# Kernel optimization log

Measured on AMD Instinct MI355X. Metric: run time of the kernel, lower is better.

The kernel has to match this reference:

```python
import jax, jax.numpy as jnp
import numpy as np
import math

N, H, E, G = 20000, 256, 320000, 1000
NF, NS = 64, 3           # sinusoid frequencies, spatial dims
DIS = 2 * NF * NS        # 384
EIN = 2 * H + 9 + DIS    # edge MLP input dim = 905


def silu(x):
    return x * jax.nn.sigmoid(x)


def sin_emb(x):
    # x: [E, 3] -> [E, 2*NF*3]
    freqs = 2.0 * math.pi * jnp.arange(NF, dtype=x.dtype)
    emb = (x[..., None] * freqs).reshape(x.shape[0], NF * NS)
    return jnp.concatenate([jnp.sin(emb), jnp.cos(emb)], axis=-1)


def layer_norm(x, gamma, beta, eps=1e-5):
    mu = jnp.mean(x, axis=-1, keepdims=True)
    var = jnp.var(x, axis=-1, keepdims=True)
    return (x - mu) * jax.lax.rsqrt(var + eps) * gamma + beta


def setup_inputs() -> dict:
    key = jax.random.key(0)
    ks = jax.random.split(key, 16)
    s = 0.02
    return {
        "node_features": jax.random.normal(ks[0], (N, H), jnp.float32),
        "lattices": jax.random.normal(ks[1], (G, 3, 3), jnp.float32),
        "edge_index": jax.random.randint(ks[2], (2, E), 0, N, dtype=jnp.int64),
        "edge2graph": jnp.sort(jax.random.randint(ks[3], (E,), 0, G, dtype=jnp.int64)),
        "frac_diff": jax.random.uniform(ks[4], (E, NS), jnp.float32),
        "num_atoms": jax.random.randint(ks[5], (G,), 0, 100, dtype=jnp.int64),
        "ln_gamma": jnp.ones((H,), jnp.float32),
        "ln_beta": jnp.zeros((H,), jnp.float32),
        "We1": jax.random.normal(ks[6], (EIN, H), jnp.float32) * s,
        "be1": jnp.zeros((H,), jnp.float32),
        "We2": jax.random.normal(ks[7], (H, H), jnp.float32) * s,
        "be2": jnp.zeros((H,), jnp.float32),
        "Wn1": jax.random.normal(ks[8], (2 * H, H), jnp.float32) * s,
        "bn1": jnp.zeros((H,), jnp.float32),
        "Wn2": jax.random.normal(ks[9], (H, H), jnp.float32) * s,
        "bn2": jnp.zeros((H,), jnp.float32),
    }


def reference(node_features, lattices, edge_index, edge2graph, frac_diff, num_atoms,
              ln_gamma, ln_beta, We1, be1, We2, be2, Wn1, bn1, Wn2, bn2):
    n = node_features.shape[0]
    h = layer_norm(node_features, ln_gamma, ln_beta)

    # edge model: gather + concat + MLP
    hi = h[edge_index[0]]                      # [E, H]
    hj = h[edge_index[1]]                      # [E, H]
    fd = sin_emb(frac_diff)                    # [E, DIS]
    ltl = jnp.einsum('gij,gkj->gik', lattices, lattices).reshape(-1, 9)  # non_symmetric: L @ L^T
    le = ltl[edge2graph]                       # [E, 9]
    x = jnp.concatenate([hi, hj, le, fd], axis=1)        # [E, EIN]
    e = silu(x @ We1 + be1)
    e = silu(e @ We2 + be2)                    # [E, H]

    # node model: scatter-mean + concat + MLP
    src = edge_index[0]
    sums = jax.ops.segment_sum(e, src, num_segments=n)   # [N, H]
    cnt = jax.ops.segment_sum(jnp.ones((e.shape[0],), e.dtype), src, num_segments=n)
    agg = sums / jnp.maximum(cnt, 1.0)[:, None]
    y = jnp.concatenate([h, agg], axis=1)                # [N, 2H]
    y = silu(y @ Wn1 + bn1)
    y = silu(y @ Wn2 + bn2)

    return node_features + y
```

## Files before the change

### kernel.cpp

```cpp
#include <hip/hip_runtime.h>

typedef unsigned short UST;
typedef __bf16 bf16x8 __attribute__((ext_vector_type(8)));
typedef float floatx4 __attribute__((ext_vector_type(4)));
typedef unsigned short ushort8v __attribute__((ext_vector_type(8)));
typedef unsigned short ushort4v __attribute__((ext_vector_type(4)));

#define N_NODES 20000
#define E_EDGES 320000
#define KF 384
#define M_PAD 20096


static __device__ __forceinline__ UST f2bf(float x){
  unsigned int u = __float_as_uint(x);
  u += 0x7fffu + ((u >> 16) & 1u);
  return (UST)(u >> 16);
}
static __device__ __forceinline__ float bf2f(UST u){
  return __uint_as_float(((unsigned int)u) << 16);
}
static __device__ __forceinline__ float siluf(float v){
  return v / (1.0f + __expf(-v));
}
static __device__ __forceinline__ unsigned int cvtpk(float lo, float hi){
  unsigned int r;
  asm("v_cvt_pk_bf16_f32 %0, %1, %2" : "=v"(r) : "v"(lo), "v"(hi));
  return r;
}
static __device__ __forceinline__ void gll16(const void* g, void* lds){
  __builtin_amdgcn_global_load_lds(
      (const __attribute__((address_space(1))) unsigned int*)g,
      (__attribute__((address_space(3))) unsigned int*)lds, 16, 0, 0);
}

static __device__ __forceinline__ void mfma_step(const UST* As, const UST* Bs,
    floatx4 (&acc)[4][4], int lm, int quad, int wM, int wN){
  bf16x8 a[4], b[4];
#pragma unroll
  for (int i = 0; i < 4; ++i)
    a[i] = *(const bf16x8*)(As + (wM + i*16 + lm)*32 + quad*8);
#pragma unroll
  for (int i = 0; i < 4; ++i)
    b[i] = *(const bf16x8*)(Bs + (wN + i*16 + lm)*32 + quad*8);
#pragma unroll
  for (int mi = 0; mi < 4; ++mi)
#pragma unroll
    for (int ni = 0; ni < 4; ++ni)
      acc[mi][ni] = __builtin_amdgcn_mfma_f32_16x16x32_bf16(a[mi], b[ni], acc[mi][ni], 0, 0, 0);
}

static __device__ __forceinline__ void mfma_stage2(const UST* At, const UST* Bg,
    int Kb, floatx4 (&acc)[4][4], int lm, int quad, int wM, int wN){
#pragma unroll 2
  for (int k0 = 0; k0 < 256; k0 += 32){
    bf16x8 a[4], b[4];
#pragma unroll
    for (int i = 0; i < 4; ++i)
      a[i] = *(const bf16x8*)(At + (wM + i*16 + lm)*264 + k0 + quad*8);
#pragma unroll
    for (int i = 0; i < 4; ++i)
      b[i] = *(const bf16x8*)(Bg + (size_t)(wN + i*16 + lm)*Kb + k0 + quad*8);
#pragma unroll
    for (int mi = 0; mi < 4; ++mi)
#pragma unroll
      for (int ni = 0; ni < 4; ++ni)
        acc[mi][ni] = __builtin_amdgcn_mfma_f32_16x16x32_bf16(a[mi], b[ni], acc[mi][ni], 0, 0, 0);
  }
}

__global__ __launch_bounds__(256) void prep_all(
    const float* __restrict__ We1, const float* __restrict__ We2,
    const float* __restrict__ Wn1, const float* __restrict__ Wn2,
    const float* __restrict__ x, const float* __restrict__ gamma,
    const float* __restrict__ beta, const float* __restrict__ lat,
    const int* __restrict__ esrc, const float* __restrict__ be1,
    int* __restrict__ cnti,
    UST* __restrict__ W1T, UST* __restrict__ W2T,
    UST* __restrict__ Wn1T, UST* __restrict__ Wn2T, UST* __restrict__ W1hT,
    UST* __restrict__ h, float* __restrict__ Pleb){
  int bid = blockIdx.x, t = threadIdx.x;
  if (bid < 384){
    int i = bid*256 + t;
    int n = i / KF, k = i % KF;
    W1T[i] = f2bf(We1[(size_t)(521 + (k&1)*192 + (k>>1))*256 + n]);
  } else if (bid < 640){
    int i = (bid-384)*256 + t;
    int n = i >> 8, k = i & 255;
    W2T[i]  = f2bf(We2[(size_t)k*256 + n]);
    Wn2T[i] = f2bf(Wn2[(size_t)k*256 + n]);
  } else if (bid < 1152){
    int i = (bid-640)*256 + t;
    int n = i >> 9, k = i & 511;
    Wn1T[i] = f2bf(Wn1[(size_t)k*256 + n]);
  } else if (bid < 1664){
    int n = bid - 1152, k = t;
    W1hT[n*256 + k] = f2bf(We1[(size_t)(k + (n & 256))*256 + (n & 255)]);
  } else if (bid < 6664){
    int wave = t >> 6, lane = t & 63;
    int row = (bid-1664)*4 + wave;
    const float4* xp = (const float4*)(x + (size_t)row * 256);
    float4 v = xp[lane];
    float s  = v.x + v.y + v.z + v.w;
    float sq = v.x*v.x + v.y*v.y + v.z*v.z + v.w*v.w;
#pragma unroll
    for (int o = 32; o > 0; o >>= 1){ s += __shfl_xor(s, o); sq += __shfl_xor(sq, o); }
    float mu  = s * (1.0f/256.0f);
    float var = sq * (1.0f/256.0f) - mu*mu;
    float rs  = rsqrtf(var + 1e-5f);
    float4 g = ((const float4*)gamma)[lane];
    float4 b = ((const float4*)beta)[lane];
    uint2 o2;
    o2.x = cvtpk((v.x-mu)*rs*g.x + b.x, (v.y-mu)*rs*g.y + b.y);
    o2.y = cvtpk((v.z-mu)*rs*g.z + b.z, (v.w-mu)*rs*g.w + b.w);
    *(uint2*)(h + (size_t)row*256 + lane*4) = o2;
  } else if (bid < 7664){
    int g = bid - 6664;
    const float* L = lat + g*9;
    float acc = be1[t];
#pragma unroll
    for (int a = 0; a < 3; ++a)
#pragma unroll
      for (int b = 0; b < 3; ++b){
        float ltlv = L[a*3+0]*L[b*3+0] + L[a*3+1]*L[b*3+1] + L[a*3+2]*L[b*3+2];
        acc += ltlv * We1[(size_t)(512 + a*3 + b)*256 + t];
      }
    int tp = (t & 0xC0) | ((t & 15) << 2) | ((t >> 4) & 3);
    Pleb[g*256 + tp] = acc;
  } else {
    int e = (bid-7664)*256 + t;
    if (e < E_EDGES) atomicAdd(&cnti[esrc[e]], 1);
  }
}

__global__ __launch_bounds__(256) void scan_kernel(const int* __restrict__ cnti,
    int* __restrict__ off, int* __restrict__ head){
  __shared__ int ps[256];
  int t = threadIdx.x;
  const int CH = 80;
  const int4* cp = (const int4*)cnti;
  int base = t * CH;
  int s = 0;
#pragma unroll 1
  for (int i = 0; i < CH/4; ++i){
    int4 v = cp[t*(CH/4) + i];
    int idx = base + i*4;
    if (idx   < N_NODES) s += v.x;
    if (idx+1 < N_NODES) s += v.y;
    if (idx+2 < N_NODES) s += v.z;
    if (idx+3 < N_NODES) s += v.w;
  }
  ps[t] = s; __syncthreads();
#pragma unroll 1
  for (int o = 1; o < 256; o <<= 1){
    int v = (t >= o) ? ps[t - o] : 0;
    __syncthreads();
    ps[t] += v;
    __syncthreads();
  }
  int run = (t > 0) ? ps[t-1] : 0;
#pragma unroll 1
  for (int i = 0; i < CH/4; ++i){
    int4 v = cp[t*(CH/4) + i];
    int idx = base + i*4;
    int a4[4] = {v.x, v.y, v.z, v.w};
#pragma unroll
    for (int j = 0; j < 4; ++j){
      int id = idx + j;
      if (id < N_NODES){ off[id] = run; head[id] = run; run += a4[j]; }
    }
  }
  if (t == 255) off[N_NODES] = run;
}

__global__ __launch_bounds__(256) void fill_kernel(const int* __restrict__ src,
    int* __restrict__ head, int* __restrict__ eidx, int* __restrict__ srcs){
  int e = blockIdx.x*256 + threadIdx.x;
  if (e < E_EDGES){
    int s = src[e];
    int p = atomicAdd(&head[s], 1);
    eidx[p] = e;
    srcs[p] = s;
  }
}

__global__ __launch_bounds__(256, 4)
void gemm_p1(const UST* __restrict__ h, const UST* __restrict__ B1,
             float* __restrict__ P1){
  __shared__ __attribute__((aligned(16))) UST lds[20480];
  UST* As0 = lds;
  UST* As1 = lds + 2048;
  UST* Bs0 = lds + 4096;
  UST* Bs1 = lds + 12288;
  int t = threadIdx.x;
  int bM = blockIdx.x >> 1, bN = (blockIdx.x & 1) << 8;
  int rA = t >> 2, cA = (t & 3) * 8;
  const UST* hrow = h + (size_t)(bM*64 + rA)*256;
  int lane = t & 63, lm = lane & 15, quad = lane >> 4;
  int wave = t >> 6, wN = wave*64;
  floatx4 acc[4][4] = {};
  UST* a0d = &As0[rA*32 + cA];
  UST* a1d = &As1[rA*32 + cA];
#pragma unroll 1
  for (int w = 0; w < 4; ++w){
    int k0 = w*64;
    gll16(hrow + k0 + cA,      a0d);
    gll16(hrow + k0 + 32 + cA, a1d);
#pragma unroll
    for (int j = 0; j < 4; ++j){
      int rB = j*64 + rA;
      gll16(B1 + (size_t)(bN + rB)*256 + k0 + cA,      &Bs0[rB*32 + cA]);
      gll16(B1 + (size_t)(bN + rB)*256 + k0 + 32 + cA, &Bs1[rB*32 + cA]);
    }
    __syncthreads();
    mfma_step(As0, Bs0, acc, lm, quad, 0, wN);
    mfma_step(As1, Bs1, acc, lm, quad, 0, wN);
    __syncthreads();
  }
  int mbase = bM*64 + quad*4;
#pragma unroll
  for (int mi = 0; mi < 4; ++mi)
#pragma unroll
    for (int r = 0; r < 4; ++r){
      int m = mbase + mi*16 + r;
      float4 v;
      v.x = acc[mi][0][r]; v.y = acc[mi][1][r];
      v.z = acc[mi][2][r]; v.w = acc[mi][3][r];
      *(float4*)(P1 + (size_t)m*512 + bN + wN + lm*4) = v;
    }
}

__global__ __launch_bounds__(512, 4)
void gemm_edge_fused(const int* __restrict__ ei, const int* __restrict__ e2g,
                     const float* __restrict__ fdif, const UST* __restrict__ W1T,
                     const int* __restrict__ eidx,
                     const UST* __restrict__ W2T, const float* __restrict__ be2,
                     const int* __restrict__ rownode,
                     const float* __restrict__ P1, const float* __restrict__ Pleb,
                     float* __restrict__ sums){
  __shared__ __attribute__((aligned(16))) UST lds[128*264];
  __shared__ int rn[128], rd[128], rg[128];
  UST* As0 = lds;
  UST* As1 = lds + 4096;
  UST* Bs0 = lds + 8192;
  UST* Bs1 = lds + 16384;
  UST* e1t = lds;
  UST* EsT = lds;
  int t = threadIdx.x;
  int bM = blockIdx.x;
  int rA = t >> 2, cA = (t & 3) * 8;
  int p0 = bM*128 + rA;
  int e0 = eidx[p0];
  float f0x = fdif[e0*3+0], f0y = fdif[e0*3+1], f0z = fdif[e0*3+2];
  size_t btb0 = (size_t)rA*KF + cA;
  size_t btb1 = btb0 + (size_t)128*KF;
  int lane = t & 63, lm = lane & 15, quad = lane >> 4;
  int wave = t >> 6, wM = (wave >> 2)*64, wN = (wave & 3)*64;
  floatx4 acc[4][4] = {};
  UST* a0d = &As0[rA*32 + cA];
  UST* a1d = &As1[rA*32 + cA];
  UST* b0d0 = &Bs0[rA*32 + cA];
  UST* b0d1 = &Bs0[(128+rA)*32 + cA];
  UST* b1d0 = &Bs1[rA*32 + cA];
  UST* b1d1 = &Bs1[(128+rA)*32 + cA];
  if (t < 128){
    int e = eidx[bM*128 + t];
    rn[t] = rownode[bM*128 + t];
    rd[t] = ei[E_EDGES + e];
    rg[t] = e2g[e];
  }

#pragma unroll 1
  for (int w = 0; w < 6; ++w){
    int k0 = w*64;
    gll16(W1T + btb0 + k0,      b0d0);
    gll16(W1T + btb1 + k0,      b0d1);
    gll16(W1T + btb0 + k0 + 32, b1d0);
    gll16(W1T + btb1 + k0 + 32, b1d1);
    int jb0 = (k0 + cA) >> 1;
    uint4 o0, o1;
    unsigned w0[4], w1[4];
#pragma unroll
    for (int ii = 0; ii < 4; ++ii){
      int jj = jb0 + ii;
      int dim = jj >> 6; float kf = (float)(jj & 63);
      float fr = (dim == 0) ? f0x : ((dim == 1) ? f0y : f0z);
      float q = __builtin_amdgcn_fractf(fr * kf);
      w0[ii] = cvtpk(__builtin_amdgcn_sinf(q), __builtin_amdgcn_cosf(q));
    }
#pragma unroll
    for (int ii = 0; ii < 4; ++ii){
      int jj = jb0 + 16 + ii;
      int dim = jj >> 6; float kf = (float)(jj & 63);
      float fr = (dim == 0) ? f0x : ((dim == 1) ? f0y : f0z);
      float q = __builtin_amdgcn_fractf(fr * kf);
      w1[ii] = cvtpk(__builtin_amdgcn_sinf(q), __builtin_amdgcn_cosf(q));
    }
    o0.x = w0[0]; o0.y = w0[1]; o0.z = w0[2]; o0.w = w0[3];
    o1.x = w1[0]; o1.y = w1[1]; o1.z = w1[2]; o1.w = w1[3];
    *(uint4*)a0d = o0;
    *(uint4*)a1d = o1;
    __syncthreads();
    mfma_step(As0, Bs0, acc, lm, quad, wM, wN);
    mfma_step(As1, Bs1, acc, lm, quad, wM, wN);
    __syncthreads();
  }

#pragma unroll
  for (int mi = 0; mi < 4; ++mi){
    int ml0 = wM + mi*16 + quad*4;
    float bs[4][4];
#pragma unroll
    for (int r = 0; r < 4; ++r){
      int ml = ml0 + r;
      float4 a4 = *(const float4*)(P1   + (size_t)rn[ml]*512 + wN + lm*4);
      float4 b4 = *(const float4*)(P1   + (size_t)rd[ml]*512 + 256 + wN + lm*4);
      float4 c4 = *(const float4*)(Pleb + (size_t)rg[ml]*256 + wN + lm*4);
      bs[r][0] = a4.x + b4.x + c4.x;
      bs[r][1] = a4.y + b4.y + c4.y;
      bs[r][2] = a4.z + b4.z + c4.z;
      bs[r][3] = a4.w + b4.w + c4.w;
    }
#pragma unroll
    for (int ni = 0; ni < 4; ++ni){
      int nl = wN + ni*16 + lm;
      float f0 = siluf(acc[mi][ni][0] + bs[0][ni]);
      float f1 = siluf(acc[mi][ni][1] + bs[1][ni]);
      float f2 = siluf(acc[mi][ni][2] + bs[2][ni]);
      float f3 = siluf(acc[mi][ni][3] + bs[3][ni]);
      unsigned w01 = cvtpk(f0, f1);
      unsigned w23 = cvtpk(f2, f3);
      e1t[(ml0+0)*264 + nl] = (UST)(w01 & 0xffffu);
      e1t[(ml0+1)*264 + nl] = (UST)(w01 >> 16);
      e1t[(ml0+2)*264 + nl] = (UST)(w23 & 0xffffu);
      e1t[(ml0+3)*264 + nl] = (UST)(w23 >> 16);
    }
  }
  __syncthreads();

  floatx4 acc2[4][4] = {};
  mfma_stage2(e1t, W2T, 256, acc2, lm, quad, wM, wN);
  __syncthreads();

#pragma unroll
  for (int mi = 0; mi < 4; ++mi)
#pragma unroll
    for (int ni = 0; ni < 4; ++ni){
      int nl = wN + ni*16 + lm;
      int ml = wM + mi*16 + quad*4;
      float b = be2[nl];
      uint2 pk2;
      pk2.x = cvtpk(siluf(acc2[mi][ni][0] + b), siluf(acc2[mi][ni][1] + b));
      pk2.y = cvtpk(siluf(acc2[mi][ni][2] + b), siluf(acc2[mi][ni][3] + b));
      *(uint2*)&EsT[nl*132 + ml] = pk2;
    }
  __syncthreads();
  {
    int c = t & 255, hh = t >> 8;
    int rbeg = hh * 64;
    int cur = rn[rbeg];
    float run = 0.0f;
#pragma unroll 1
    for (int r = rbeg; r < rbeg + 64; r += 4){
      ushort4v v4 = *(const ushort4v*)&EsT[c*132 + r];
#pragma unroll
      for (int q2 = 0; q2 < 4; ++q2){
        int nd = rn[r + q2];
        if (nd != cur){ atomicAdd(&sums[(size_t)cur*256 + c], run); run = 0.0f; cur = nd; }
        run += bf2f(v4[q2]);
      }
    }
    atomicAdd(&sums[(size_t)cur*256 + c], run);
  }
}

__global__ __launch_bounds__(256, 4)
void gemm_node12(const UST* __restrict__ h, const float* __restrict__ sums,
                 const int* __restrict__ offs, const UST* __restrict__ B1,
                 const float* __restrict__ bn1, const UST* __restrict__ B2,
                 const float* __restrict__ bn2,
                 float* __restrict__ out_f, const float* __restrict__ resid){
  __shared__ __attribute__((aligned(16))) UST lds[20480];
  UST* As0 = lds;
  UST* As1 = lds + 2048;
  UST* Bs0 = lds + 4096;
  UST* Bs1 = lds + 12288;
  UST* y1t = lds;
  int t = threadIdx.x;
  int bM = blockIdx.x;
  int rA = t >> 2, cA = (t & 3) * 8;
  int row = bM*64 + rA;
  bool valid = row < N_NODES;
  float inv = 0.0f;
  if (valid){
    int deg = offs[row+1] - offs[row];
    inv = 1.0f / fmaxf((float)deg, 1.0f);
  }
  const UST* hrow = h + (size_t)row*256;
  const float* srow = sums + (size_t)row*256;
  int lane = t & 63, lm = lane & 15, quad = lane >> 4;
  int wave = t >> 6, wN = wave*64;
  floatx4 acc[4][4] = {};
  UST* a0d = &As0[rA*32 + cA];
  UST* a1d = &As1[rA*32 + cA];
  const uint4 z4 = {0,0,0,0};
#pragma unroll 1
  for (int w = 0; w < 8; ++w){
    int k0 = w*64;
    if (k0 < 256){
      if (valid){
        gll16(hrow + k0 + cA,      a0d);
        gll16(hrow + k0 + 32 + cA, a1d);
      } else {
        *(uint4*)a0d = z4;
        *(uint4*)a1d = z4;
      }
    } else {
      uint4 o0 = z4, o1 = z4;
      if (valid){
        int q = k0 - 256 + cA;
        float4 s0 = *(const float4*)(srow + q);
        float4 s1 = *(const float4*)(srow + q + 4);
        o0.x = cvtpk(s0.x*inv, s0.y*inv); o0.y = cvtpk(s0.z*inv, s0.w*inv);
        o0.z = cvtpk(s1.x*inv, s1.y*inv); o0.w = cvtpk(s1.z*inv, s1.w*inv);
        float4 s2 = *(const float4*)(srow + q + 32);
        float4 s3 = *(const float4*)(srow + q + 36);
        o1.x = cvtpk(s2.x*inv, s2.y*inv); o1.y = cvtpk(s2.z*inv, s2.w*inv);
        o1.z = cvtpk(s3.x*inv, s3.y*inv); o1.w = cvtpk(s3.z*inv, s3.w*inv);
      }
      *(uint4*)a0d = o0;
      *(uint4*)a1d = o1;
    }
#pragma unroll
    for (int j = 0; j < 4; ++j){
      int rB = j*64 + rA;
      gll16(B1 + (size_t)rB*512 + k0 + cA,      &Bs0[rB*32 + cA]);
      gll16(B1 + (size_t)rB*512 + k0 + 32 + cA, &Bs1[rB*32 + cA]);
    }
    __syncthreads();
    mfma_step(As0, Bs0, acc, lm, quad, 0, wN);
    mfma_step(As1, Bs1, acc, lm, quad, 0, wN);
    __syncthreads();
  }
#pragma unroll
  for (int mi = 0; mi < 4; ++mi){
    int ml0 = mi*16 + quad*4;
#pragma unroll
    for (int ni = 0; ni < 4; ++ni){
      int nl = wN + ni*16 + lm;
      float b = bn1[nl];
      unsigned w01 = cvtpk(siluf(acc[mi][ni][0] + b), siluf(acc[mi][ni][1] + b));
      unsigned w23 = cvtpk(siluf(acc[mi][ni][2] + b), siluf(acc[mi][ni][3] + b));
      y1t[(ml0+0)*264 + nl] = (UST)(w01 & 0xffffu);
      y1t[(ml0+1)*264 + nl] = (UST)(w01 >> 16);
      y1t[(ml0+2)*264 + nl] = (UST)(w23 & 0xffffu);
      y1t[(ml0+3)*264 + nl] = (UST)(w23 >> 16);
    }
  }
  __syncthreads();
  floatx4 acc2[4][4] = {};
  mfma_stage2(y1t, B2, 256, acc2, lm, quad, 0, wN);
  int mbase = bM*64 + quad*4;
  int nbase = wN + lm;
#pragma unroll
  for (int mi = 0; mi < 4; ++mi)
#pragma unroll
    for (int r = 0; r < 4; ++r){
      int m = mbase + mi*16 + r;
      if (m < N_NODES){
#pragma unroll
        for (int ni = 0; ni < 4; ++ni){
          int n = nbase + ni*16;
          float v = siluf(acc2[mi][ni][r] + bn2[n]);
          out_f[(size_t)m*256 + n] = resid[(size_t)m*256 + n] + v;
        }
      }
    }
}

extern "C" void kernel_launch(void* const* d_in, const int* in_sizes, int n_in,
                              void* d_out, int out_size, void* d_ws, size_t ws_size,
                              hipStream_t stream){
  (void)in_sizes; (void)n_in; (void)out_size; (void)ws_size;
  const float* node_features = (const float*)d_in[0];
  const float* lattices      = (const float*)d_in[1];
  const int*   edge_index    = (const int*)d_in[2];
  const int*   edge2graph    = (const int*)d_in[3];
  const float* frac_diff     = (const float*)d_in[4];
  const float* ln_gamma      = (const float*)d_in[6];
  const float* ln_beta       = (const float*)d_in[7];
  const float* We1 = (const float*)d_in[8];
  const float* be1 = (const float*)d_in[9];
  const float* We2 = (const float*)d_in[10];
  const float* be2 = (const float*)d_in[11];
  const float* Wn1 = (const float*)d_in[12];
  const float* bn1 = (const float*)d_in[13];
  const float* Wn2 = (const float*)d_in[14];
  const float* bn2 = (const float*)d_in[15];

  char* w = (char*)d_ws;
  size_t off_b = 0;
  auto carve = [&](size_t bytes) -> char* {
    char* p = w + off_b; off_b += (bytes + 1023) & ~(size_t)1023; return p;
  };
  UST*   W1T  = (UST*)carve((size_t)256*KF*2);
  UST*   W2T  = (UST*)carve((size_t)256*256*2);
  UST*   Wn1T = (UST*)carve((size_t)256*512*2);
  UST*   Wn2T = (UST*)carve((size_t)256*256*2);
  UST*   W1hT = (UST*)carve((size_t)512*256*2);
  UST*   hbf  = (UST*)carve((size_t)M_PAD*256*2);
  float* P1   = (float*)carve((size_t)M_PAD*512*4);
  float* Pleb = (float*)carve((size_t)1000*256*4);
  int*   cnti = (int*)carve((size_t)20480*4);
  int*   offs = (int*)carve((size_t)(N_NODES+1)*4);
  int*   head = (int*)carve((size_t)N_NODES*4);
  int*   eidx = (int*)carve((size_t)E_EDGES*4);
  int*   srcs = (int*)carve((size_t)E_EDGES*4);
  float* sums = (float*)carve((size_t)N_NODES*256*4);

  hipMemsetAsync(cnti, 0, (size_t)20480*4, stream);
  hipMemsetAsync(sums, 0, (size_t)N_NODES*256*4, stream);

  prep_all<<<7664 + E_EDGES/256, 256, 0, stream>>>(We1, We2, Wn1, Wn2,
      node_features, ln_gamma, ln_beta, lattices, edge_index, be1, cnti,
      W1T, W2T, Wn1T, Wn2T, W1hT, hbf, Pleb);

  scan_kernel<<<1, 256, 0, stream>>>(cnti, offs, head);
  fill_kernel<<<E_EDGES/256, 256, 0, stream>>>(edge_index, head, eidx, srcs);

  gemm_p1<<<(M_PAD/64)*2, 256, 0, stream>>>(hbf, W1hT, P1);

  gemm_edge_fused<<<E_EDGES/128, 512, 0, stream>>>(
      edge_index, edge2graph, frac_diff, W1T, eidx, W2T, be2, srcs, P1, Pleb, sums);

  gemm_node12<<<M_PAD/64, 256, 0, stream>>>(
      hbf, sums, offs, Wn1T, bn1, Wn2T, bn2, (float*)d_out, node_features);
}
```

Before: 437.4 us.

## Double-buffer sinusoid GEMM K-loop and use angle-addition for sin/cos

Restructures the fused edge GEMM's K loop from 6 steps of 64 into 12 steps of 32 with ping-pong LDS buffers. The A tile (sin/cos embedding) and the W1 B tile for the next step are built and loaded while MFMAs run on the current buffer, so there is one barrier per step instead of two. The four consecutive sin/cos pairs are now produced with angle-addition recurrences from one hardware sin/cos call, which cuts transcendental work but adds some rounding drift. SiLU also switches from division to a reciprocal-multiply.

```diff
diff --git a/kernel.cpp b/kernel.cpp
--- a/kernel.cpp
+++ b/kernel.cpp
@@ -21,7 +21,7 @@
   return __uint_as_float(((unsigned int)u) << 16);
 }
 static __device__ __forceinline__ float siluf(float v){
-  return v / (1.0f + __expf(-v));
+  return v * __builtin_amdgcn_rcpf(1.0f + __expf(-v));
 }
 static __device__ __forceinline__ unsigned int cvtpk(float lo, float hi){
   unsigned int r;
@@ -240,10 +240,10 @@
                      float* __restrict__ sums){
   __shared__ __attribute__((aligned(16))) UST lds[128*264];
   __shared__ int rn[128], rd[128], rg[128];
-  UST* As0 = lds;
-  UST* As1 = lds + 4096;
-  UST* Bs0 = lds + 8192;
-  UST* Bs1 = lds + 16384;
+  UST* Ab0 = lds;
+  UST* Ab1 = lds + 4096;
+  UST* Bb0 = lds + 8192;
+  UST* Bb1 = lds + 16384;
   UST* e1t = lds;
   UST* EsT = lds;
   int t = threadIdx.x;
@@ -257,12 +257,6 @@
   int lane = t & 63, lm = lane & 15, quad = lane >> 4;
   int wave = t >> 6, wM = (wave >> 2)*64, wN = (wave & 3)*64;
   floatx4 acc[4][4] = {};
-  UST* a0d = &As0[rA*32 + cA];
-  UST* a1d = &As1[rA*32 + cA];
-  UST* b0d0 = &Bs0[rA*32 + cA];
-  UST* b0d1 = &Bs0[(128+rA)*32 + cA];
-  UST* b1d0 = &Bs1[rA*32 + cA];
-  UST* b1d1 = &Bs1[(128+rA)*32 + cA];
   if (t < 128){
     int e = eidx[bM*128 + t];
     rn[t] = rownode[bM*128 + t];
@@ -270,39 +264,49 @@
     rg[t] = e2g[e];
   }
 
-#pragma unroll 1
-  for (int w = 0; w < 6; ++w){
-    int k0 = w*64;
-    gll16(W1T + btb0 + k0,      b0d0);
-    gll16(W1T + btb1 + k0,      b0d1);
-    gll16(W1T + btb0 + k0 + 32, b1d0);
-    gll16(W1T + btb1 + k0 + 32, b1d1);
-    int jb0 = (k0 + cA) >> 1;
-    uint4 o0, o1;
-    unsigned w0[4], w1[4];
-#pragma unroll
-    for (int ii = 0; ii < 4; ++ii){
-      int jj = jb0 + ii;
-      int dim = jj >> 6; float kf = (float)(jj & 63);
-      float fr = (dim == 0) ? f0x : ((dim == 1) ? f0y : f0z);
-      float q = __builtin_amdgcn_fractf(fr * kf);
-      w0[ii] = cvtpk(__builtin_amdgcn_sinf(q), __builtin_amdgcn_cosf(q));
-    }
-#pragma unroll
-    for (int ii = 0; ii < 4; ++ii){
-      int jj = jb0 + 16 + ii;
-      int dim = jj >> 6; float kf = (float)(jj & 63);
-      float fr = (dim == 0) ? f0x : ((dim == 1) ? f0y : f0z);
-      float q = __builtin_amdgcn_fractf(fr * kf);
-      w1[ii] = cvtpk(__builtin_amdgcn_sinf(q), __builtin_amdgcn_cosf(q));
-    }
-    o0.x = w0[0]; o0.y = w0[1]; o0.z = w0[2]; o0.w = w0[3];
-    o1.x = w1[0]; o1.y = w1[1]; o1.z = w1[2]; o1.w = w1[3];
-    *(uint4*)a0d = o0;
-    *(uint4*)a1d = o1;
-    __syncthreads();
-    mfma_step(As0, Bs0, acc, lm, quad, wM, wN);
-    mfma_step(As1, Bs1, acc, lm, quad, wM, wN);
+  float sdx = __builtin_amdgcn_sinf(f0x), cdx = __builtin_amdgcn_cosf(f0x);
+  float sdy = __builtin_amdgcn_sinf(f0y), cdy = __builtin_amdgcn_cosf(f0y);
+  float sdz = __builtin_amdgcn_sinf(f0z), cdz = __builtin_amdgcn_cosf(f0z);
+
+  auto buildA = [&](int s)->uint4 {
+    int j0 = s*16 + (cA >> 1);
+    int dim = j0 >> 6;
+    float fr = (dim == 0) ? f0x : ((dim == 1) ? f0y : f0z);
+    float sd = (dim == 0) ? sdx : ((dim == 1) ? sdy : sdz);
+    float cd = (dim == 0) ? cdx : ((dim == 1) ? cdy : cdz);
+    float q  = __builtin_amdgcn_fractf(fr * (float)(j0 & 63));
+    float sn = __builtin_amdgcn_sinf(q);
+    float cs = __builtin_amdgcn_cosf(q);
+    uint4 o;
+    o.x = cvtpk(sn, cs);
+    float s2;
+    s2 = fmaf(sn, cd, cs*sd); cs = fmaf(cs, cd, -sn*sd); sn = s2; o.y = cvtpk(sn, cs);
+    s2 = fmaf(sn, cd, cs*sd); cs = fmaf(cs, cd, -sn*sd); sn = s2; o.z = cvtpk(sn, cs);
+    s2 = fmaf(sn, cd, cs*sd); cs = fmaf(cs, cd, -sn*sd); sn = s2; o.w = cvtpk(sn, cs);
+    return o;
+  };
+
+  {
+    uint4 o = buildA(0);
+    *(uint4*)&Ab0[rA*32 + cA] = o;
+    gll16(W1T + btb0, &Bb0[rA*32 + cA]);
+    gll16(W1T + btb1, &Bb0[(128+rA)*32 + cA]);
+  }
+  __syncthreads();
+#pragma unroll 1
+  for (int s = 0; s < 12; ++s){
+    UST* Ac = (s & 1) ? Ab1 : Ab0;
+    UST* Bc = (s & 1) ? Bb1 : Bb0;
+    if (s < 11){
+      uint4 o = buildA(s+1);
+      UST* An = (s & 1) ? Ab0 : Ab1;
+      UST* Bn = (s & 1) ? Bb0 : Bb1;
+      *(uint4*)&An[rA*32 + cA] = o;
+      int k0 = (s+1)*32;
+      gll16(W1T + btb0 + k0, &Bn[rA*32 + cA]);
+      gll16(W1T + btb1 + k0, &Bn[(128+rA)*32 + cA]);
+    }
+    mfma_step(Ac, Bc, acc, lm, quad, wM, wN);
     __syncthreads();
   }
 
```

After: 488.1 us. 11.6% more time.
